# Kernel optimization log

Hardware: AMD Instinct MI355X
Metric: run time of the kernel (lower is better)

The kernel has to match this reference:

```python
import jax, jax.numpy as jnp
import numpy as np

D_MODEL = 256
N_HEADS = 8
HEAD_DIM = D_MODEL // N_HEADS  # 32
N_LEVELS = 4
N_POINTS = 4
LEVEL_SHAPES = [(100, 100), (50, 50), (25, 25), (13, 13)]
LEVEL_STARTS = [0] + list(np.cumsum([h * w for h, w in LEVEL_SHAPES]))[:-1]
LEN_IN = int(sum(h * w for h, w in LEVEL_SHAPES))  # 13294
BATCH = 2
LEN_Q = LEN_IN  # encoder self-attention


def _offset_bias():
    # faithful to MSDeformAttn._reset_parameters for sampling_offsets bias
    thetas = np.arange(N_HEADS, dtype=np.float32) * (2.0 * np.pi / N_HEADS)
    grid = np.stack([np.cos(thetas), np.sin(thetas)], -1)
    grid = grid / np.abs(grid).max(-1, keepdims=True)
    grid = np.tile(grid.reshape(N_HEADS, 1, 1, 2), (1, N_LEVELS, N_POINTS, 1))
    for i in range(N_POINTS):
        grid[:, :, i, :] *= i + 1
    return jnp.asarray(grid.reshape(-1), dtype=jnp.float32)


def setup_inputs() -> dict:
    key = jax.random.key(0)
    ks = jax.random.split(key, 10)
    s = 1.0 / np.sqrt(D_MODEL)
    inp = {
        "query": jax.random.normal(ks[0], (BATCH, LEN_Q, D_MODEL), jnp.float32),
        "reference_points": jax.random.uniform(ks[1], (BATCH, LEN_Q, N_LEVELS, 2), jnp.float32),
        "input_flatten": jax.random.normal(ks[2], (BATCH, LEN_IN, D_MODEL), jnp.float32),
        "input_spatial_shapes": jnp.asarray(LEVEL_SHAPES, dtype=jnp.int32),
        "W_value": jax.random.normal(ks[3], (D_MODEL, D_MODEL), jnp.float32) * s,
        "b_value": jnp.zeros((D_MODEL,), jnp.float32),
        "W_off": jax.random.normal(ks[4], (D_MODEL, N_HEADS * N_LEVELS * N_POINTS * 2), jnp.float32) * 0.01,
        "b_off": _offset_bias(),
        "W_attn": jax.random.normal(ks[5], (D_MODEL, N_HEADS * N_LEVELS * N_POINTS), jnp.float32) * 0.01,
        "b_attn": jnp.zeros((N_HEADS * N_LEVELS * N_POINTS,), jnp.float32),
        "W_out": jax.random.normal(ks[6], (D_MODEL, D_MODEL), jnp.float32) * s,
        "b_out": jnp.zeros((D_MODEL,), jnp.float32),
    }
    return inp


def _corner(v_t, ix, iy, h, w):
    # v_t: (n, M, h*w, D); ix/iy: (n, M, LqP) int32. Zero padding outside.
    valid = (ix >= 0) & (ix < w) & (iy >= 0) & (iy < h)
    idx = jnp.clip(iy, 0, h - 1) * w + jnp.clip(ix, 0, w - 1)
    g = jnp.take_along_axis(v_t, idx[..., None], axis=2)  # (n, M, LqP, D)
    return g * valid[..., None].astype(v_t.dtype)


def _ms_deform_attn(query, reference_points, input_flatten,
                    W_value, b_value, W_off, b_off, W_attn, b_attn, W_out, b_out):
    n, lq, _ = query.shape
    value = (input_flatten @ W_value + b_value).reshape(n, LEN_IN, N_HEADS, HEAD_DIM)
    offs = (query @ W_off + b_off).reshape(n, lq, N_HEADS, N_LEVELS, N_POINTS, 2)
    aw = jax.nn.softmax(
        (query @ W_attn + b_attn).reshape(n, lq, N_HEADS, N_LEVELS * N_POINTS), axis=-1
    ).reshape(n, lq, N_HEADS, N_LEVELS, N_POINTS)
    # offset_normalizer = (w, h) per level
    norm = jnp.asarray([[w, h] for h, w in LEVEL_SHAPES], dtype=query.dtype)
    loc = reference_points[:, :, None, :, None, :] + offs / norm[None, None, None, :, None, :]

    acc = jnp.zeros((n, N_HEADS, lq, HEAD_DIM), dtype=value.dtype)
    for l, (h, w) in enumerate(LEVEL_SHAPES):
        s0 = LEVEL_STARTS[l]
        v_t = jnp.transpose(value[:, s0:s0 + h * w], (0, 2, 1, 3))  # (n, M, hw, D)
        ll = loc[:, :, :, l]  # (n, lq, M, P, 2) in [0,1]
        # grid_sample bilinear, align_corners=False: pixel = coord*size - 0.5
        x = ll[..., 0] * w - 0.5
        y = ll[..., 1] * h - 0.5
        x0 = jnp.floor(x); y0 = jnp.floor(y)
        tx = x - x0; ty = y - y0
        ix0 = x0.astype(jnp.int32); iy0 = y0.astype(jnp.int32)
        flat = lambda a: jnp.transpose(a, (0, 2, 1, 3)).reshape(n, N_HEADS, lq * N_POINTS)
        ix0f, iy0f = flat(ix0), flat(iy0)
        txf = flat(tx)[..., None]; tyf = flat(ty)[..., None]
        g00 = _corner(v_t, ix0f, iy0f, h, w)
        g01 = _corner(v_t, ix0f + 1, iy0f, h, w)
        g10 = _corner(v_t, ix0f, iy0f + 1, h, w)
        g11 = _corner(v_t, ix0f + 1, iy0f + 1, h, w)
        samp = (g00 * (1 - txf) * (1 - tyf) + g01 * txf * (1 - tyf)
                + g10 * (1 - txf) * tyf + g11 * txf * tyf)
        samp = samp.reshape(n, N_HEADS, lq, N_POINTS, HEAD_DIM)
        wl = jnp.transpose(aw[:, :, :, l], (0, 2, 1, 3))[..., None]  # (n, M, lq, P, 1)
        acc = acc + (samp * wl).sum(axis=3)

    out = jnp.transpose(acc, (0, 2, 1, 3)).reshape(n, lq, D_MODEL)
    return out @ W_out + b_out


def reference(query, reference_points, input_flatten, input_spatial_shapes,
              W_value, b_value, W_off, b_off, W_attn, b_attn, W_out, b_out):
    # input_spatial_shapes carried for signature fidelity; level geometry is static.
    return _ms_deform_attn(query, reference_points, input_flatten,
                           W_value, b_value, W_off, b_off, W_attn, b_attn, W_out, b_out)
```

## Files before the change

### kernel.cpp

```cpp
#include <hip/hip_runtime.h>

#define NH 8
#define HD 32
#define NL 4
#define NP 4
#define DM 256
#define LEN_IN_C 13294
#define LQ_C 13294
#define B_C 2
#define M_TOTAL (B_C * LQ_C)
#define MT_TILES 1662

typedef __attribute__((ext_vector_type(8))) short short8;
typedef __attribute__((ext_vector_type(4))) float floatx4;

__device__ __forceinline__ unsigned short f2bf(float x) {
    union { float f; unsigned int u; } a; a.f = x;
    unsigned int r = (a.u + 0x7FFFu + ((a.u >> 16) & 1u)) >> 16;
    return (unsigned short)r;
}
__device__ __forceinline__ float bflo(unsigned int u) {
    union { unsigned int u; float f; } a; a.u = u << 16; return a.f;
}
__device__ __forceinline__ float bfhi(unsigned int u) {
    union { unsigned int u; float f; } a; a.u = u & 0xffff0000u; return a.f;
}

__global__ __launch_bounds__(256) void conv_a_kernel(const float* __restrict__ A0,
                                                     unsigned short* __restrict__ D0,
                                                     const float* __restrict__ A1,
                                                     unsigned short* __restrict__ D1,
                                                     int M) {
    const float* A = blockIdx.y ? A1 : A0;
    unsigned short* Asw = blockIdx.y ? D1 : D0;
    const int u = blockIdx.x * 256 + threadIdx.x;
    const int lane = u & 63;
    const int kc = (u >> 6) & 7;
    const int rt = u >> 9;
    const int row = rt * 16 + (lane & 15);
    const int col0 = kc * 32 + (lane >> 4) * 8;
    unsigned short tmp[8];
    if (row < M) {
        const float4 f0 = *(const float4*)(A + (size_t)row * 256 + col0);
        const float4 f1 = *(const float4*)(A + (size_t)row * 256 + col0 + 4);
        tmp[0] = f2bf(f0.x); tmp[1] = f2bf(f0.y); tmp[2] = f2bf(f0.z); tmp[3] = f2bf(f0.w);
        tmp[4] = f2bf(f1.x); tmp[5] = f2bf(f1.y); tmp[6] = f2bf(f1.z); tmp[7] = f2bf(f1.w);
    } else {
#pragma unroll
        for (int j = 0; j < 8; ++j) tmp[j] = 0;
    }
    short8 v;
#pragma unroll
    for (int j = 0; j < 8; ++j) v[j] = (short)tmp[j];
    ((short8*)Asw)[u] = v;
}

__device__ __forceinline__ void conv_b_body(const float* __restrict__ W,
                                            unsigned short* __restrict__ Bsw,
                                            int Nsrc, int NTsrc, int NTtotal, int ntOff,
                                            int vblk) {
    const int u = vblk * 256 + threadIdx.x;
    const int lane = u & 63;
    const int unit = u >> 6;
    const int ntl = unit % NTsrc;
    const int kc = unit / NTsrc;
    const int n = ntl * 16 + (lane & 15);
    const int k0 = kc * 32 + (lane >> 4) * 8;
    short8 v;
#pragma unroll
    for (int j = 0; j < 8; ++j)
        v[j] = (short)f2bf(W[(size_t)(k0 + j) * Nsrc + n]);
    ((short8*)Bsw)[(size_t)(kc * NTtotal + ntOff + ntl) * 64 + lane] = v;
}

__global__ __launch_bounds__(256) void conv_weights_kernel(const float* __restrict__ Wv,
                                                           const float* __restrict__ Woff,
                                                           const float* __restrict__ Wattn,
                                                           const float* __restrict__ Wout,
                                                           const float* __restrict__ boff,
                                                           const float* __restrict__ battn,
                                                           unsigned short* __restrict__ BswV,
                                                           unsigned short* __restrict__ BswOA,
                                                           unsigned short* __restrict__ BswO,
                                                           float* __restrict__ fbias) {
    const int blk = blockIdx.x;
    if (blk < 32)        conv_b_body(Wv,    BswV,  256, 16, 16, 0,  blk);
    else if (blk < 64)   conv_b_body(Woff,  BswOA, 256, 16, 24, 0,  blk - 32);
    else if (blk < 80)   conv_b_body(Wattn, BswOA, 128,  8, 24, 16, blk - 64);
    else if (blk < 112)  conv_b_body(Wout,  BswO,  256, 16, 16, 0,  blk - 80);
    else {
        const int t = (blk - 112) * 256 + threadIdx.x;
        if (t < 384) fbias[t] = (t < 256) ? boff[t] : battn[t - 256];
    }
}

template <int NT, bool OUT_BF16>
__global__ __launch_bounds__(256) void mfma_gemm_kernel(const unsigned short* __restrict__ Asw,
                                                        const unsigned short* __restrict__ Bsw,
                                                        const float* __restrict__ bias,
                                                        void* __restrict__ Cout, int M) {
    constexpr int NTW = NT / 4;
    const int tid = threadIdx.x;
    const int lane = tid & 63;
    const int wave = tid >> 6;
    const int rt0 = blockIdx.x * 2;

    const short8* Au = (const short8*)Asw;
    const short8* Bu = (const short8*)Bsw;

    floatx4 acc[2][NTW];
#pragma unroll
    for (int r = 0; r < 2; ++r)
#pragma unroll
        for (int t = 0; t < NTW; ++t) acc[r][t] = (floatx4){0.f, 0.f, 0.f, 0.f};

#pragma unroll 2
    for (int kc = 0; kc < 8; ++kc) {
        const short8 a0 = Au[(size_t)(rt0 * 8 + kc) * 64 + lane];
        const short8 a1 = Au[(size_t)((rt0 + 1) * 8 + kc) * 64 + lane];
#pragma unroll
        for (int t = 0; t < NTW; ++t) {
            const short8 b = Bu[(size_t)(kc * NT + wave * NTW + t) * 64 + lane];
            acc[0][t] = __builtin_amdgcn_mfma_f32_16x16x32_bf16(a0, b, acc[0][t], 0, 0, 0);
            acc[1][t] = __builtin_amdgcn_mfma_f32_16x16x32_bf16(a1, b, acc[1][t], 0, 0, 0);
        }
    }

    const int N = NT * 16;
    const int colq = lane & 15;
    const int rowq = (lane >> 4) * 4;
#pragma unroll
    for (int t = 0; t < NTW; ++t) {
        const int col = (wave * NTW + t) * 16 + colq;
        const float bc = bias[col];
#pragma unroll
        for (int r = 0; r < 2; ++r) {
            const int rowb = (rt0 + r) * 16 + rowq;
#pragma unroll
            for (int reg = 0; reg < 4; ++reg) {
                const int row = rowb + reg;
                if (row < M) {
                    const float v = acc[r][t][reg] + bc;
                    if (OUT_BF16)
                        ((unsigned short*)Cout)[(size_t)row * N + col] = f2bf(v);
                    else
                        ((float*)Cout)[(size_t)row * N + col] = v;
                }
            }
        }
    }
}

__global__ __launch_bounds__(256, 6) void msda_sample_kernel(const float* __restrict__ refp,
                                                             const unsigned short* __restrict__ value,
                                                             const float* __restrict__ fused,
                                                             unsigned short* __restrict__ AccSw) {
    constexpr int lvl_hw[4] = {100, 50, 25, 13};
    constexpr int lvl_s[4] = {0, 10000, 12500, 13125};

    const int bq0 = blockIdx.x * 4;
    const int tid = threadIdx.x;

    __shared__ float s_ref[32];
    __shared__ int4 s_pi[4 * 8 * 17];
    __shared__ float4 s_pw[4 * 8 * 17];

    if (tid < 32) s_ref[tid] = refp[(size_t)bq0 * 8 + tid];
    __syncthreads();

#pragma unroll
    for (int jj = 0; jj < 2; ++jj) {
        const int job = jj * 256 + tid;
        const int qq = job >> 7;
        const int t = job & 127;
        const int h = t >> 4;
        const int l = (t >> 2) & 3;
        const int bq = bq0 + qq;
        const int b = (bq >= LQ_C) ? 1 : 0;

        const float logit = fused[(size_t)bq * 384 + 256 + t];
        float m = logit;
#pragma unroll
        for (int mask = 1; mask < 16; mask <<= 1) m = fmaxf(m, __shfl_xor(m, mask));
        const float e = expf(logit - m);
        float s = e;
#pragma unroll
        for (int mask = 1; mask < 16; mask <<= 1) s += __shfl_xor(s, mask);
        const float aw = e / s;

        const int whl = lvl_hw[l];
        const float fwh = (float)whl;
        const float2 oxy = *(const float2*)(fused + (size_t)bq * 384 + t * 2);
        const float x = s_ref[qq * 8 + l * 2] * fwh + oxy.x - 0.5f;
        const float y = s_ref[qq * 8 + l * 2 + 1] * fwh + oxy.y - 0.5f;
        const float x0f = floorf(x), y0f = floorf(y);
        const float tx = x - x0f, ty = y - y0f;
        const int ix0 = (int)x0f, iy0 = (int)y0f;

        const bool xv0 = (unsigned)ix0 < (unsigned)whl;
        const bool xv1 = (unsigned)(ix0 + 1) < (unsigned)whl;
        const bool yv0 = (unsigned)iy0 < (unsigned)whl;
        const bool yv1 = (unsigned)(iy0 + 1) < (unsigned)whl;

        const int cx0 = min(max(ix0, 0), whl - 1);
        const int cx1 = min(max(ix0 + 1, 0), whl - 1);
        const int cy0 = min(max(iy0, 0), whl - 1);
        const int cy1 = min(max(iy0 + 1, 0), whl - 1);

        const int base = (b * LEN_IN_C + lvl_s[l]) * 256 + h * 32;
        const int r0 = base + cy0 * (whl * 256);
        const int r1 = base + cy1 * (whl * 256);
        int4 ii;
        ii.x = (r0 + cx0 * 256) * 2;
        ii.y = (r0 + cx1 * 256) * 2;
        ii.z = (r1 + cx0 * 256) * 2;
        ii.w = (r1 + cx1 * 256) * 2;
        float4 wv;
        wv.x = (xv0 && yv0) ? aw * (1.f - tx) * (1.f - ty) : 0.f;
        wv.y = (xv1 && yv0) ? aw * tx * (1.f - ty) : 0.f;
        wv.z = (xv0 && yv1) ? aw * (1.f - tx) * ty : 0.f;
        wv.w = (xv1 && yv1) ? aw * tx * ty : 0.f;
        const int slot = (qq * 8 + h) * 17 + (t & 15);
        s_pi[slot] = ii;
        s_pw[slot] = wv;
    }
    __syncthreads();

    const int qq = tid >> 6;
    const int h = (tid >> 3) & 7;
    const int l8 = tid & 7;
    const int d4 = l8 * 8;
    const char* vb = (const char*)value;
    const int pbase = (qq * 8 + h) * 17;

    float4 acc0 = {0.f, 0.f, 0.f, 0.f};
    float4 acc1 = {0.f, 0.f, 0.f, 0.f};
#pragma unroll 2
    for (int pt = 0; pt < 16; ++pt) {
        const int4 ii = s_pi[pbase + pt];
        const float4 wv = s_pw[pbase + pt];
        const uint2 v00 = *(const uint2*)(vb + (ii.x + d4));
        const uint2 v01 = *(const uint2*)(vb + (ii.y + d4));
        const uint2 v10 = *(const uint2*)(vb + (ii.z + d4));
        const uint2 v11 = *(const uint2*)(vb + (ii.w + d4));
        acc0.x += wv.x * bflo(v00.x); acc0.y += wv.x * bfhi(v00.x);
        acc0.z += wv.x * bflo(v00.y); acc0.w += wv.x * bfhi(v00.y);
        acc1.x += wv.y * bflo(v01.x); acc1.y += wv.y * bfhi(v01.x);
        acc1.z += wv.y * bflo(v01.y); acc1.w += wv.y * bfhi(v01.y);
        acc0.x += wv.z * bflo(v10.x); acc0.y += wv.z * bfhi(v10.x);
        acc0.z += wv.z * bflo(v10.y); acc0.w += wv.z * bfhi(v10.y);
        acc1.x += wv.w * bflo(v11.x); acc1.y += wv.w * bfhi(v11.x);
        acc1.z += wv.w * bflo(v11.y); acc1.w += wv.w * bfhi(v11.y);
    }
    const float4 acc = {acc0.x + acc1.x, acc0.y + acc1.y, acc0.z + acc1.z, acc0.w + acc1.w};

    const int bq = bq0 + qq;
    const int rt = bq >> 4, mm = bq & 15;
    const int col = h * 32 + l8 * 4;
    const int kc = col >> 5, q2 = (col >> 3) & 3, j = col & 7;
    unsigned int p0 = (unsigned int)f2bf(acc.x) | ((unsigned int)f2bf(acc.y) << 16);
    unsigned int p1 = (unsigned int)f2bf(acc.z) | ((unsigned int)f2bf(acc.w) << 16);
    uint2 pk; pk.x = p0; pk.y = p1;
    *(uint2*)(AccSw + ((size_t)((rt * 8 + kc) * 64 + (q2 * 16 + mm)) * 8 + j)) = pk;
}

extern "C" void kernel_launch(void* const* d_in, const int* in_sizes, int n_in,
                              void* d_out, int out_size, void* d_ws, size_t ws_size,
                              hipStream_t stream) {
    const float* query  = (const float*)d_in[0];
    const float* refp   = (const float*)d_in[1];
    const float* inflat = (const float*)d_in[2];
    const float* Wv    = (const float*)d_in[4];
    const float* bv    = (const float*)d_in[5];
    const float* Woff  = (const float*)d_in[6];
    const float* boff  = (const float*)d_in[7];
    const float* Wattn = (const float*)d_in[8];
    const float* battn = (const float*)d_in[9];
    const float* Wout  = (const float*)d_in[10];
    const float* bout  = (const float*)d_in[11];
    float* out = (float*)d_out;

    char* p = (char*)d_ws;
    const size_t aswBytes = (size_t)MT_TILES * 8 * 64 * 8 * sizeof(unsigned short);
    unsigned short* AswQ = (unsigned short*)p;           p += aswBytes;
    unsigned short* AswS = (unsigned short*)p;           p += aswBytes;
    unsigned short* BswV = (unsigned short*)p;           p += (size_t)8 * 16 * 64 * 8 * 2;
    unsigned short* BswOA = (unsigned short*)p;          p += (size_t)8 * 24 * 64 * 8 * 2;
    unsigned short* BswO = (unsigned short*)p;           p += (size_t)8 * 16 * 64 * 8 * 2;
    float* fbias = (float*)p;                            p += 384 * sizeof(float);
    unsigned short* value = (unsigned short*)p;          p += (size_t)M_TOTAL * 256 * 2;
    float* fused = (float*)p;                            p += (size_t)M_TOTAL * 384 * 4;

    const int M = M_TOTAL;

    conv_weights_kernel<<<114, 256, 0, stream>>>(Wv, Woff, Wattn, Wout, boff, battn,
                                                 BswV, BswOA, BswO, fbias);
    conv_a_kernel<<<dim3(MT_TILES * 2, 2), 256, 0, stream>>>(inflat, AswS, query, AswQ, M);

    const int gemmBlocks = MT_TILES / 2;
    mfma_gemm_kernel<16, true><<<gemmBlocks, 256, 0, stream>>>(AswS, BswV, bv, value, M);
    mfma_gemm_kernel<24, false><<<gemmBlocks, 256, 0, stream>>>(AswQ, BswOA, fbias, fused, M);
    msda_sample_kernel<<<M / 4, 256, 0, stream>>>(refp, value, fused, AswS);
    mfma_gemm_kernel<16, false><<<gemmBlocks, 256, 0, stream>>>(AswS, BswO, bout, out, M);
}
```

Baseline: 230.7 us.

## Fuse fp32-to-bf16 conversion into GEMMs and re-layout value for paired-corner sampling

Drops the separate activation-conversion kernel: the value and offset/attention GEMMs now load fp32 rows directly and convert to bf16 in registers with a packed convert instruction. The value projection is written in a head-major (batch, head, position, 32) layout with zero padding around it, so each sampling thread loads 16 bytes covering two horizontally adjacent corners. That halves the per-point index storage and load count, and a shuffle combines the left and right halves. Occupancy is raised to 8 waves per SIMD. The cost is scattered 2-byte stores in the value GEMM epilogue and redundant fp32 reads of A across waves.

```diff
diff --git a/kernel.cpp b/kernel.cpp
--- a/kernel.cpp
+++ b/kernel.cpp
@@ -13,46 +13,22 @@
 
 typedef __attribute__((ext_vector_type(8))) short short8;
 typedef __attribute__((ext_vector_type(4))) float floatx4;
+typedef __attribute__((ext_vector_type(2))) float floatx2;
 
 __device__ __forceinline__ unsigned short f2bf(float x) {
     union { float f; unsigned int u; } a; a.f = x;
     unsigned int r = (a.u + 0x7FFFu + ((a.u >> 16) & 1u)) >> 16;
     return (unsigned short)r;
 }
-__device__ __forceinline__ float bflo(unsigned int u) {
-    union { unsigned int u; float f; } a; a.u = u << 16; return a.f;
-}
-__device__ __forceinline__ float bfhi(unsigned int u) {
-    union { unsigned int u; float f; } a; a.u = u & 0xffff0000u; return a.f;
-}
-
-__global__ __launch_bounds__(256) void conv_a_kernel(const float* __restrict__ A0,
-                                                     unsigned short* __restrict__ D0,
-                                                     const float* __restrict__ A1,
-                                                     unsigned short* __restrict__ D1,
-                                                     int M) {
-    const float* A = blockIdx.y ? A1 : A0;
-    unsigned short* Asw = blockIdx.y ? D1 : D0;
-    const int u = blockIdx.x * 256 + threadIdx.x;
-    const int lane = u & 63;
-    const int kc = (u >> 6) & 7;
-    const int rt = u >> 9;
-    const int row = rt * 16 + (lane & 15);
-    const int col0 = kc * 32 + (lane >> 4) * 8;
-    unsigned short tmp[8];
-    if (row < M) {
-        const float4 f0 = *(const float4*)(A + (size_t)row * 256 + col0);
-        const float4 f1 = *(const float4*)(A + (size_t)row * 256 + col0 + 4);
-        tmp[0] = f2bf(f0.x); tmp[1] = f2bf(f0.y); tmp[2] = f2bf(f0.z); tmp[3] = f2bf(f0.w);
-        tmp[4] = f2bf(f1.x); tmp[5] = f2bf(f1.y); tmp[6] = f2bf(f1.z); tmp[7] = f2bf(f1.w);
-    } else {
-#pragma unroll
-        for (int j = 0; j < 8; ++j) tmp[j] = 0;
-    }
-    short8 v;
-#pragma unroll
-    for (int j = 0; j < 8; ++j) v[j] = (short)tmp[j];
-    ((short8*)Asw)[u] = v;
+__device__ __forceinline__ floatx2 up2(unsigned int u) {
+    union { unsigned int u; float f; } lo, hi;
+    lo.u = u << 16; hi.u = u & 0xffff0000u;
+    floatx2 r; r.x = lo.f; r.y = hi.f; return r;
+}
+__device__ __forceinline__ unsigned int cvtpk_bf16(float lo, float hi) {
+    unsigned int r;
+    asm("v_cvt_pk_bf16_f32 %0, %1, %2" : "=v"(r) : "v"(lo), "v"(hi));
+    return r;
 }
 
 __device__ __forceinline__ void conv_b_body(const float* __restrict__ W,
@@ -82,15 +58,106 @@
                                                            unsigned short* __restrict__ BswV,
                                                            unsigned short* __restrict__ BswOA,
                                                            unsigned short* __restrict__ BswO,
-                                                           float* __restrict__ fbias) {
+                                                           float* __restrict__ fbias,
+                                                           unsigned short* __restrict__ value,
+                                                           unsigned short* __restrict__ AccSw) {
     const int blk = blockIdx.x;
     if (blk < 32)        conv_b_body(Wv,    BswV,  256, 16, 16, 0,  blk);
     else if (blk < 64)   conv_b_body(Woff,  BswOA, 256, 16, 24, 0,  blk - 32);
     else if (blk < 80)   conv_b_body(Wattn, BswOA, 128,  8, 24, 16, blk - 64);
     else if (blk < 112)  conv_b_body(Wout,  BswO,  256, 16, 16, 0,  blk - 80);
-    else {
+    else if (blk < 114) {
         const int t = (blk - 112) * 256 + threadIdx.x;
         if (t < 384) fbias[t] = (t < 256) ? boff[t] : battn[t - 256];
+        else if (t < 416) {
+            const int j = t - 384;
+            value[-32 + j] = 0;
+            value[(size_t)M_TOTAL * 256 + j] = 0;
+        }
+    } else {
+        const int idx = threadIdx.x;
+        if (idx < 128) {
+            const int kc = idx >> 4;
+            const int sub = idx & 15;
+            const int lane = (12 + (sub & 3)) + 16 * (sub >> 2);
+            const size_t unit = (size_t)(1661 * 8 + kc) * 64 + lane;
+            short8 z = (short8){0, 0, 0, 0, 0, 0, 0, 0};
+            ((short8*)AccSw)[unit] = z;
+        }
+    }
+}
+
+template <int NT, int OUTMODE>
+__global__ __launch_bounds__(256) void mfma_gemm_f32a(const float* __restrict__ A,
+                                                      const unsigned short* __restrict__ Bsw,
+                                                      const float* __restrict__ bias,
+                                                      void* __restrict__ Cout, int M) {
+    constexpr int NTW = NT / 4;
+    const int tid = threadIdx.x;
+    const int lane = tid & 63;
+    const int wave = tid >> 6;
+    const int rt0 = blockIdx.x * 2;
+    const int m = lane & 15;
+    const int q = lane >> 4;
+
+    const float* Ar0 = A + (size_t)min(rt0 * 16 + m, M - 1) * 256 + q * 8;
+    const float* Ar1 = A + (size_t)min(rt0 * 16 + 16 + m, M - 1) * 256 + q * 8;
+    const short8* Bu = (const short8*)Bsw;
+
+    floatx4 acc[2][NTW];
+#pragma unroll
+    for (int r = 0; r < 2; ++r)
+#pragma unroll
+        for (int t = 0; t < NTW; ++t) acc[r][t] = (floatx4){0.f, 0.f, 0.f, 0.f};
+
+#pragma unroll 2
+    for (int kc = 0; kc < 8; ++kc) {
+        const float4 f00 = *(const float4*)(Ar0 + kc * 32);
+        const float4 f01 = *(const float4*)(Ar0 + kc * 32 + 4);
+        const float4 f10 = *(const float4*)(Ar1 + kc * 32);
+        const float4 f11 = *(const float4*)(Ar1 + kc * 32 + 4);
+        union { uint4 u; short8 s; } c0, c1;
+        c0.u.x = cvtpk_bf16(f00.x, f00.y); c0.u.y = cvtpk_bf16(f00.z, f00.w);
+        c0.u.z = cvtpk_bf16(f01.x, f01.y); c0.u.w = cvtpk_bf16(f01.z, f01.w);
+        c1.u.x = cvtpk_bf16(f10.x, f10.y); c1.u.y = cvtpk_bf16(f10.z, f10.w);
+        c1.u.z = cvtpk_bf16(f11.x, f11.y); c1.u.w = cvtpk_bf16(f11.z, f11.w);
+        const short8 a0 = c0.s;
+        const short8 a1 = c1.s;
+#pragma unroll
+        for (int t = 0; t < NTW; ++t) {
+            const short8 b = Bu[(size_t)(kc * NT + wave * NTW + t) * 64 + lane];
+            acc[0][t] = __builtin_amdgcn_mfma_f32_16x16x32_bf16(a0, b, acc[0][t], 0, 0, 0);
+            acc[1][t] = __builtin_amdgcn_mfma_f32_16x16x32_bf16(a1, b, acc[1][t], 0, 0, 0);
+        }
+    }
+
+    const int N = NT * 16;
+    const int colq = lane & 15;
+    const int rowq = (lane >> 4) * 4;
+#pragma unroll
+    for (int t = 0; t < NTW; ++t) {
+        const int col = (wave * NTW + t) * 16 + colq;
+        const float bc = bias[col];
+#pragma unroll
+        for (int r = 0; r < 2; ++r) {
+            const int rowb = (rt0 + r) * 16 + rowq;
+#pragma unroll
+            for (int reg = 0; reg < 4; ++reg) {
+                const int row = rowb + reg;
+                if (row < M) {
+                    const float v = acc[r][t][reg] + bc;
+                    if (OUTMODE == 1) {
+                        const int bb = row >= LEN_IN_C;
+                        const int pos = row - (bb ? LEN_IN_C : 0);
+                        const int hh = col >> 5;
+                        const int dd = col & 31;
+                        ((unsigned short*)Cout)[((size_t)((bb << 3) + hh) * LEN_IN_C + pos) * 32 + dd] = f2bf(v);
+                    } else {
+                        ((float*)Cout)[(size_t)row * N + col] = v;
+                    }
+                }
+            }
+        }
     }
 }
 
@@ -151,7 +218,7 @@
     }
 }
 
-__global__ __launch_bounds__(256, 6) void msda_sample_kernel(const float* __restrict__ refp,
+__global__ __launch_bounds__(256, 8) void msda_sample_kernel(const float* __restrict__ refp,
                                                              const unsigned short* __restrict__ value,
                                                              const float* __restrict__ fused,
                                                              unsigned short* __restrict__ AccSw) {
@@ -162,7 +229,7 @@
     const int tid = threadIdx.x;
 
     __shared__ float s_ref[32];
-    __shared__ int4 s_pi[4 * 8 * 17];
+    __shared__ int2 s_pi[4 * 8 * 17];
     __shared__ float4 s_pw[4 * 8 * 17];
 
     if (tid < 32) s_ref[tid] = refp[(size_t)bq0 * 8 + tid];
@@ -202,26 +269,21 @@
         const bool yv0 = (unsigned)iy0 < (unsigned)whl;
         const bool yv1 = (unsigned)(iy0 + 1) < (unsigned)whl;
 
-        const int cx0 = min(max(ix0, 0), whl - 1);
-        const int cx1 = min(max(ix0 + 1, 0), whl - 1);
+        const int cxp = min(max(ix0, -1), whl - 1);
         const int cy0 = min(max(iy0, 0), whl - 1);
         const int cy1 = min(max(iy0 + 1, 0), whl - 1);
 
-        const int base = (b * LEN_IN_C + lvl_s[l]) * 256 + h * 32;
-        const int r0 = base + cy0 * (whl * 256);
-        const int r1 = base + cy1 * (whl * 256);
-        int4 ii;
-        ii.x = (r0 + cx0 * 256) * 2;
-        ii.y = (r0 + cx1 * 256) * 2;
-        ii.z = (r1 + cx0 * 256) * 2;
-        ii.w = (r1 + cx1 * 256) * 2;
+        const int posb = (b * 8 + h) * LEN_IN_C + lvl_s[l];
+        int2 aa;
+        aa.x = (posb + cy0 * whl + cxp) * 64;
+        aa.y = (posb + cy1 * whl + cxp) * 64;
         float4 wv;
         wv.x = (xv0 && yv0) ? aw * (1.f - tx) * (1.f - ty) : 0.f;
         wv.y = (xv1 && yv0) ? aw * tx * (1.f - ty) : 0.f;
         wv.z = (xv0 && yv1) ? aw * (1.f - tx) * ty : 0.f;
         wv.w = (xv1 && yv1) ? aw * tx * ty : 0.f;
         const int slot = (qq * 8 + h) * 17 + (t & 15);
-        s_pi[slot] = ii;
+        s_pi[slot] = aa;
         s_pw[slot] = wv;
     }
     __syncthreads();
@@ -229,39 +291,49 @@
     const int qq = tid >> 6;
     const int h = (tid >> 3) & 7;
     const int l8 = tid & 7;
-    const int d4 = l8 * 8;
-    const char* vb = (const char*)value;
+    const char* vbp = (const char*)value + l8 * 16;
     const int pbase = (qq * 8 + h) * 17;
-
-    float4 acc0 = {0.f, 0.f, 0.f, 0.f};
-    float4 acc1 = {0.f, 0.f, 0.f, 0.f};
+    const bool right = (l8 & 4) != 0;
+
+    floatx2 acc0 = (floatx2){0.f, 0.f}, acc1 = acc0, acc2 = acc0, acc3 = acc0;
 #pragma unroll 2
     for (int pt = 0; pt < 16; ++pt) {
-        const int4 ii = s_pi[pbase + pt];
+        const int2 aa = s_pi[pbase + pt];
         const float4 wv = s_pw[pbase + pt];
-        const uint2 v00 = *(const uint2*)(vb + (ii.x + d4));
-        const uint2 v01 = *(const uint2*)(vb + (ii.y + d4));
-        const uint2 v10 = *(const uint2*)(vb + (ii.z + d4));
-        const uint2 v11 = *(const uint2*)(vb + (ii.w + d4));
-        acc0.x += wv.x * bflo(v00.x); acc0.y += wv.x * bfhi(v00.x);
-        acc0.z += wv.x * bflo(v00.y); acc0.w += wv.x * bfhi(v00.y);
-        acc1.x += wv.y * bflo(v01.x); acc1.y += wv.y * bfhi(v01.x);
-        acc1.z += wv.y * bflo(v01.y); acc1.w += wv.y * bfhi(v01.y);
-        acc0.x += wv.z * bflo(v10.x); acc0.y += wv.z * bfhi(v10.x);
-        acc0.z += wv.z * bflo(v10.y); acc0.w += wv.z * bfhi(v10.y);
-        acc1.x += wv.w * bflo(v11.x); acc1.y += wv.w * bfhi(v11.x);
-        acc1.z += wv.w * bflo(v11.y); acc1.w += wv.w * bfhi(v11.y);
-    }
-    const float4 acc = {acc0.x + acc1.x, acc0.y + acc1.y, acc0.z + acc1.z, acc0.w + acc1.w};
-
-    const int bq = bq0 + qq;
-    const int rt = bq >> 4, mm = bq & 15;
-    const int col = h * 32 + l8 * 4;
-    const int kc = col >> 5, q2 = (col >> 3) & 3, j = col & 7;
-    unsigned int p0 = (unsigned int)f2bf(acc.x) | ((unsigned int)f2bf(acc.y) << 16);
-    unsigned int p1 = (unsigned int)f2bf(acc.z) | ((unsigned int)f2bf(acc.w) << 16);
-    uint2 pk; pk.x = p0; pk.y = p1;
-    *(uint2*)(AccSw + ((size_t)((rt * 8 + kc) * 64 + (q2 * 16 + mm)) * 8 + j)) = pk;
+        const float wt = right ? wv.y : wv.x;
+        const float wb = right ? wv.w : wv.z;
+        const uint4 vt = *(const uint4*)(vbp + aa.x);
+        const uint4 vbm = *(const uint4*)(vbp + aa.y);
+        const floatx2 w2t = (floatx2){wt, wt};
+        const floatx2 w2b = (floatx2){wb, wb};
+        acc0 += w2t * up2(vt.x);
+        acc1 += w2t * up2(vt.y);
+        acc2 += w2t * up2(vt.z);
+        acc3 += w2t * up2(vt.w);
+        acc0 += w2b * up2(vbm.x);
+        acc1 += w2b * up2(vbm.y);
+        acc2 += w2b * up2(vbm.z);
+        acc3 += w2b * up2(vbm.w);
+    }
+
+    float r0 = acc0.x, r1 = acc0.y, r2 = acc1.x, r3 = acc1.y;
+    float r4 = acc2.x, r5 = acc2.y, r6 = acc3.x, r7 = acc3.y;
+    r0 += __shfl_xor(r0, 4); r1 += __shfl_xor(r1, 4);
+    r2 += __shfl_xor(r2, 4); r3 += __shfl_xor(r3, 4);
+    r4 += __shfl_xor(r4, 4); r5 += __shfl_xor(r5, 4);
+    r6 += __shfl_xor(r6, 4); r7 += __shfl_xor(r7, 4);
+
+    if (!right) {
+        const int bq = bq0 + qq;
+        const int rt = bq >> 4, mm = bq & 15;
+        const int unit = (rt * 8 + h) * 64 + ((l8 & 3) * 16 + mm);
+        uint4 o;
+        o.x = cvtpk_bf16(r0, r1);
+        o.y = cvtpk_bf16(r2, r3);
+        o.z = cvtpk_bf16(r4, r5);
+        o.w = cvtpk_bf16(r6, r7);
+        *(uint4*)(AccSw + (size_t)unit * 8) = o;
+    }
 }
 
 extern "C" void kernel_launch(void* const* d_in, const int* in_sizes, int n_in,
@@ -281,25 +353,23 @@
     float* out = (float*)d_out;
 
     char* p = (char*)d_ws;
-    const size_t aswBytes = (size_t)MT_TILES * 8 * 64 * 8 * sizeof(unsigned short);
-    unsigned short* AswQ = (unsigned short*)p;           p += aswBytes;
-    unsigned short* AswS = (unsigned short*)p;           p += aswBytes;
-    unsigned short* BswV = (unsigned short*)p;           p += (size_t)8 * 16 * 64 * 8 * 2;
-    unsigned short* BswOA = (unsigned short*)p;          p += (size_t)8 * 24 * 64 * 8 * 2;
-    unsigned short* BswO = (unsigned short*)p;           p += (size_t)8 * 16 * 64 * 8 * 2;
-    float* fbias = (float*)p;                            p += 384 * sizeof(float);
-    unsigned short* value = (unsigned short*)p;          p += (size_t)M_TOTAL * 256 * 2;
-    float* fused = (float*)p;                            p += (size_t)M_TOTAL * 384 * 4;
+    unsigned short* AccSw = (unsigned short*)p;
+    p += (size_t)MT_TILES * 8 * 64 * 8 * sizeof(unsigned short);
+    unsigned short* BswV = (unsigned short*)p;   p += (size_t)8 * 16 * 64 * 8 * 2;
+    unsigned short* BswOA = (unsigned short*)p;  p += (size_t)8 * 24 * 64 * 8 * 2;
+    unsigned short* BswO = (unsigned short*)p;   p += (size_t)8 * 16 * 64 * 8 * 2;
+    float* fbias = (float*)p;                    p += 384 * sizeof(float);
+    unsigned short* value = (unsigned short*)p + 32;
+    p += ((size_t)M_TOTAL * 256 + 64) * sizeof(unsigned short);
+    float* fused = (float*)p;                    p += (size_t)M_TOTAL * 384 * 4;
 
     const int M = M_TOTAL;
-
-    conv_weights_kernel<<<114, 256, 0, stream>>>(Wv, Woff, Wattn, Wout, boff, battn,
-                                                 BswV, BswOA, BswO, fbias);
-    conv_a_kernel<<<dim3(MT_TILES * 2, 2), 256, 0, stream>>>(inflat, AswS, query, AswQ, M);
-
     const int gemmBlocks = MT_TILES / 2;
-    mfma_gemm_kernel<16, true><<<gemmBlocks, 256, 0, stream>>>(AswS, BswV, bv, value, M);
-    mfma_gemm_kernel<24, false><<<gemmBlocks, 256, 0, stream>>>(AswQ, BswOA, fbias, fused, M);
-    msda_sample_kernel<<<M / 4, 256, 0, stream>>>(refp, value, fused, AswS);
-    mfma_gemm_kernel<16, false><<<gemmBlocks, 256, 0, stream>>>(AswS, BswO, bout, out, M);
-}
+
+    conv_weights_kernel<<<115, 256, 0, stream>>>(Wv, Woff, Wattn, Wout, boff, battn,
+                                                 BswV, BswOA, BswO, fbias, value, AccSw);
+    mfma_gemm_f32a<16, 1><<<gemmBlocks, 256, 0, stream>>>(inflat, BswV, bv, value, M);
+    mfma_gemm_f32a<24, 0><<<gemmBlocks, 256, 0, stream>>>(query, BswOA, fbias, fused, M);
+    msda_sample_kernel<<<M / 4, 256, 0, stream>>>(refp, value, fused, AccSw);
+    mfma_gemm_kernel<16, false><<<gemmBlocks, 256, 0, stream>>>(AccSw, BswO, bout, out, M);
+}
```

Measured after the change: 226.1 us. 2.0% less time.
